# Kernel optimization log

Measured on AMD Instinct MI355X. Metric: run time of the kernel, lower is better.

## Reference

```python
import jax, jax.numpy as jnp
import numpy as np

P_IN = 32  # MODEL_CONFIG['p_in']; note: all 32 sample points share the same offsets in the source


def _bilinear_border(feat, sx, sy):
    """Replicates F.grid_sample(mode='bilinear', padding_mode='border', align_corners=False)
    for a single point per (b, n). feat: [B,C,H,W]; sx, sy: [B,N] in pixel coords.
    align_corners=False unnormalization of grid built as 2*s/size - 1 gives px = s - 0.5.
    Returns [B,N,C]."""
    H, W = feat.shape[-2], feat.shape[-1]
    px = jnp.clip(sx - 0.5, 0.0, W - 1.0)  # border padding clamps coords
    py = jnp.clip(sy - 0.5, 0.0, H - 1.0)
    x0 = jnp.floor(px)
    y0 = jnp.floor(py)
    wx = (px - x0)[..., None]  # [B,N,1]
    wy = (py - y0)[..., None]
    x0i = x0.astype(jnp.int32)
    y0i = y0.astype(jnp.int32)
    x1i = jnp.minimum(x0i + 1, W - 1)
    y1i = jnp.minimum(y0i + 1, H - 1)

    def gather(f, yi, xi):  # f [C,H,W], yi/xi [N] -> [N,C]
        return f[:, yi, xi].T

    g = jax.vmap(gather)  # over batch
    v00 = g(feat, y0i, x0i)
    v01 = g(feat, y0i, x1i)
    v10 = g(feat, y1i, x0i)
    v11 = g(feat, y1i, x1i)
    return (v00 * (1 - wx) * (1 - wy) + v01 * wx * (1 - wy)
            + v10 * (1 - wx) * wy + v11 * wx * wy)


def _forward(feats, query_pos, query_content, W_off, b_off, sigma_z):
    offsets = query_content @ W_off + b_off  # [B,N,3]
    x, y, z, r = (query_pos[..., i] for i in range(4))
    dx, dy, dz = offsets[..., 0], offsets[..., 1], offsets[..., 2]
    sx = x + dx * (2.0 ** (z - r))
    sy = y + dy * (2.0 ** (z + r))
    sz = z + dz
    L = len(feats)
    levels = jnp.arange(L, dtype=sz.dtype)
    # gaussian z weight, then softmax over levels (as in source: softmax of the exp values)
    w = jnp.exp(-((sz[..., None] - levels) ** 2) / (2.0 * sigma_z ** 2))  # [B,N,L]
    zw = jax.nn.softmax(w, axis=-1)
    out = sum(zw[..., l:l + 1] * _bilinear_border(feats[l], sx, sy) for l in range(L))  # [B,N,C]
    B, N, C = out.shape
    # all P_IN sample points use identical coords in the source -> broadcast
    return jnp.broadcast_to(out[:, :, None, :], (B, N, P_IN, C))


def setup_inputs() -> dict:
    key = jax.random.key(0)
    ks = jax.random.split(key, 8)
    B, N, C = 8, 300, 256
    sizes = [(100, 100), (50, 50), (25, 25), (13, 13)]
    feats = [jax.random.normal(ks[i], (B, C, h, w), dtype=jnp.float32)
             for i, (h, w) in enumerate(sizes)]
    u = jax.random.uniform(ks[4], (B, N, 4), dtype=jnp.float32)
    # x in [0,100), y in [0,100) (level-0 pixel coords), z in [0,4), r in [0,1)
    query_pos = u * jnp.array([100.0, 100.0, 4.0, 1.0], dtype=jnp.float32)
    query_content = jax.random.normal(ks[5], (B, N, C), dtype=jnp.float32)
    W_off = jax.random.normal(ks[6], (C, 3), dtype=jnp.float32) * 0.02
    b_off = jnp.zeros((3,), dtype=jnp.float32)
    sigma_z = jnp.ones((1,), dtype=jnp.float32) * 0.5
    return {"feat0": feats[0], "feat1": feats[1], "feat2": feats[2], "feat3": feats[3],
            "query_pos": query_pos, "query_content": query_content,
            "W_off": W_off, "b_off": b_off, "sigma_z": sigma_z}


def reference(feat0, feat1, feat2, feat3, query_pos, query_content, W_off, b_off, sigma_z):
    return _forward([feat0, feat1, feat2, feat3], query_pos, query_content, W_off, b_off, sigma_z)
```

## Files before the change

### kernel.cpp

```cpp
#include <hip/hip_runtime.h>

constexpr int Bc = 8;
constexpr int Nc = 300;
constexpr int Cc = 256;
constexpr int Pc = 32;

__global__ __launch_bounds__(256) void sampling3d_kernel(
    const float* __restrict__ f0, const float* __restrict__ f1,
    const float* __restrict__ f2, const float* __restrict__ f3,
    const float* __restrict__ qpos, const float* __restrict__ qcont,
    const float* __restrict__ Woff, const float* __restrict__ boff,
    const float* __restrict__ sigma, float* __restrict__ out)
{
    const int q = blockIdx.x;
    const int b = q / Nc;
    const int c = threadIdx.x;

    float qc = qcont[q * Cc + c];
    float p0 = qc * Woff[c * 3 + 0];
    float p1 = qc * Woff[c * 3 + 1];
    float p2 = qc * Woff[c * 3 + 2];
#pragma unroll
    for (int off = 32; off > 0; off >>= 1) {
        p0 += __shfl_down(p0, off, 64);
        p1 += __shfl_down(p1, off, 64);
        p2 += __shfl_down(p2, off, 64);
    }
    __shared__ float red[4][3];
    __shared__ float par[8];
    const int wave = threadIdx.x >> 6;
    const int lane = threadIdx.x & 63;
    if (lane == 0) { red[wave][0] = p0; red[wave][1] = p1; red[wave][2] = p2; }
    __syncthreads();
    if (threadIdx.x == 0) {
        float dx = red[0][0] + red[1][0] + red[2][0] + red[3][0] + boff[0];
        float dy = red[0][1] + red[1][1] + red[2][1] + red[3][1] + boff[1];
        float dz = red[0][2] + red[1][2] + red[2][2] + red[3][2] + boff[2];
        float x = qpos[q * 4 + 0];
        float y = qpos[q * 4 + 1];
        float z = qpos[q * 4 + 2];
        float r = qpos[q * 4 + 3];
        float sx = x + dx * exp2f(z - r);
        float sy = y + dy * exp2f(z + r);
        float sz = z + dz;
        float sg = sigma[0];
        float inv = 1.0f / (2.0f * sg * sg);
        float e[4];
        float s = 0.f;
#pragma unroll
        for (int l = 0; l < 4; ++l) {
            float d = sz - (float)l;
            float w = expf(-d * d * inv);
            e[l] = expf(w);
            s += e[l];
        }
        float rs = 1.0f / s;
        par[0] = sx;
        par[1] = sy;
#pragma unroll
        for (int l = 0; l < 4; ++l) par[2 + l] = e[l] * rs;
    }
    __syncthreads();

    const float sx = par[0];
    const float sy = par[1];

    const float* const fs[4] = {f0, f1, f2, f3};
    const int HWs[4] = {100, 50, 25, 13};

    float acc = 0.f;
#pragma unroll
    for (int l = 0; l < 4; ++l) {
        const int H = HWs[l];
        const int W = HWs[l];
        const float zw = par[2 + l];
        float px = fminf(fmaxf(sx - 0.5f, 0.f), (float)(W - 1));
        float py = fminf(fmaxf(sy - 0.5f, 0.f), (float)(H - 1));
        float x0f = floorf(px);
        float y0f = floorf(py);
        float wx = px - x0f;
        float wy = py - y0f;
        int x0 = (int)x0f;
        int y0 = (int)y0f;
        int x1 = min(x0 + 1, W - 1);
        int y1 = min(y0 + 1, H - 1);
        const float* base = fs[l] + (size_t)((b * Cc + c) * H) * W;
        float v00 = base[y0 * W + x0];
        float v01 = base[y0 * W + x1];
        float v10 = base[y1 * W + x0];
        float v11 = base[y1 * W + x1];
        float top = v00 + wx * (v01 - v00);
        float bot = v10 + wx * (v11 - v10);
        acc += zw * (top + wy * (bot - top));
    }

    float* o = out + (size_t)q * (Pc * Cc) + c;
#pragma unroll
    for (int p = 0; p < Pc; ++p) o[p * Cc] = acc;
}

extern "C" void kernel_launch(void* const* d_in, const int* in_sizes, int n_in,
                              void* d_out, int out_size, void* d_ws, size_t ws_size,
                              hipStream_t stream) {
    const float* f0    = (const float*)d_in[0];
    const float* f1    = (const float*)d_in[1];
    const float* f2    = (const float*)d_in[2];
    const float* f3    = (const float*)d_in[3];
    const float* qpos  = (const float*)d_in[4];
    const float* qcont = (const float*)d_in[5];
    const float* Woff  = (const float*)d_in[6];
    const float* boff  = (const float*)d_in[7];
    const float* sigma = (const float*)d_in[8];
    float* out = (float*)d_out;

    sampling3d_kernel<<<Bc * Nc, 256, 0, stream>>>(
        f0, f1, f2, f3, qpos, qcont, Woff, boff, sigma, out);
}
```

Baseline: 195.5 us.

## Split into params, LDS-staged per-channel sampling, and vectorized broadcast kernels

Splits the fused kernel into three launches. The first computes per-query sample coordinates and level weights into workspace. The second stages each (batch, channel) feature pyramid in LDS and samples all 300 queries from it, writing a transposed intermediate. The third broadcasts the result to the 32 sample points using 16-byte nontemporal stores. The aim is to replace scattered global gathers with LDS reads and to vectorize the large output write, at the cost of two extra launches, a workspace round-trip, and an original path kept as fallback.

```diff
diff --git a/kernel.cpp b/kernel.cpp
--- a/kernel.cpp
+++ b/kernel.cpp
@@ -5,17 +5,20 @@
 constexpr int Cc = 256;
 constexpr int Pc = 32;
 
-__global__ __launch_bounds__(256) void sampling3d_kernel(
-    const float* __restrict__ f0, const float* __restrict__ f1,
-    const float* __restrict__ f2, const float* __restrict__ f3,
+typedef float f32x4 __attribute__((ext_vector_type(4)));
+
+__constant__ int c_HW[4] = {100, 50, 25, 13};
+constexpr int LVL_N[4]   = {10000, 2500, 625, 169};
+constexpr int LVL_OFF[4] = {0, 10000, 12500, 13125};
+constexpr int LDS_FLOATS = 13294;
+
+__global__ __launch_bounds__(256) void params_kernel(
     const float* __restrict__ qpos, const float* __restrict__ qcont,
     const float* __restrict__ Woff, const float* __restrict__ boff,
-    const float* __restrict__ sigma, float* __restrict__ out)
+    const float* __restrict__ sigma, float* __restrict__ params)
 {
     const int q = blockIdx.x;
-    const int b = q / Nc;
     const int c = threadIdx.x;
-
     float qc = qcont[q * Cc + c];
     float p0 = qc * Woff[c * 3 + 0];
     float p1 = qc * Woff[c * 3 + 1];
@@ -27,10 +30,10 @@
         p2 += __shfl_down(p2, off, 64);
     }
     __shared__ float red[4][3];
-    __shared__ float par[8];
     const int wave = threadIdx.x >> 6;
-    const int lane = threadIdx.x & 63;
-    if (lane == 0) { red[wave][0] = p0; red[wave][1] = p1; red[wave][2] = p2; }
+    if ((threadIdx.x & 63) == 0) {
+        red[wave][0] = p0; red[wave][1] = p1; red[wave][2] = p2;
+    }
     __syncthreads();
     if (threadIdx.x == 0) {
         float dx = red[0][0] + red[1][0] + red[2][0] + red[3][0] + boff[0];
@@ -50,53 +53,186 @@
 #pragma unroll
         for (int l = 0; l < 4; ++l) {
             float d = sz - (float)l;
-            float w = expf(-d * d * inv);
-            e[l] = expf(w);
+            float w = __expf(-d * d * inv);
+            e[l] = __expf(w);
             s += e[l];
         }
         float rs = 1.0f / s;
-        par[0] = sx;
-        par[1] = sy;
+        params[q * 8 + 0] = sx;
+        params[q * 8 + 1] = sy;
+#pragma unroll
+        for (int l = 0; l < 4; ++l) params[q * 8 + 2 + l] = e[l] * rs;
+    }
+}
+
+__global__ __launch_bounds__(256) void sample_kernel(
+    const float* __restrict__ f0, const float* __restrict__ f1,
+    const float* __restrict__ f2, const float* __restrict__ f3,
+    const float* __restrict__ params, float* __restrict__ outT)
+{
+    __shared__ float sl[LDS_FLOATS];
+    const int bc = blockIdx.x;
+    const int t = threadIdx.x;
+
+    {
+        const f32x4* src = (const f32x4*)(f0 + (size_t)bc * 10000);
+        f32x4* dst = (f32x4*)&sl[LVL_OFF[0]];
+        for (int i = t; i < 2500; i += 256) dst[i] = src[i];
+    }
+    {
+        const f32x4* src = (const f32x4*)(f1 + (size_t)bc * 2500);
+        f32x4* dst = (f32x4*)&sl[LVL_OFF[1]];
+        for (int i = t; i < 625; i += 256) dst[i] = src[i];
+    }
+    {
+        const float* src = f2 + (size_t)bc * 625;
+        float* dst = &sl[LVL_OFF[2]];
+        for (int i = t; i < 625; i += 256) dst[i] = src[i];
+    }
+    {
+        const float* src = f3 + (size_t)bc * 169;
+        float* dst = &sl[LVL_OFF[3]];
+        if (t < 169) dst[t] = src[t];
+    }
+    __syncthreads();
+
+    const int b = bc >> 8;
+    for (int n = t; n < Nc; n += 256) {
+        const int q = b * Nc + n;
+        const float sx = params[q * 8 + 0];
+        const float sy = params[q * 8 + 1];
+        float acc = 0.f;
+#pragma unroll
+        for (int l = 0; l < 4; ++l) {
+            const int W = c_HW[l];
+            const float zw = params[q * 8 + 2 + l];
+            float px = fminf(fmaxf(sx - 0.5f, 0.f), (float)(W - 1));
+            float py = fminf(fmaxf(sy - 0.5f, 0.f), (float)(W - 1));
+            float x0f = floorf(px);
+            float y0f = floorf(py);
+            float wx = px - x0f;
+            float wy = py - y0f;
+            int x0 = (int)x0f;
+            int y0 = (int)y0f;
+            int x1 = min(x0 + 1, W - 1);
+            int y1 = min(y0 + 1, W - 1);
+            const float* base = &sl[LVL_OFF[l]];
+            float v00 = base[y0 * W + x0];
+            float v01 = base[y0 * W + x1];
+            float v10 = base[y1 * W + x0];
+            float v11 = base[y1 * W + x1];
+            float top = v00 + wx * (v01 - v00);
+            float bot = v10 + wx * (v11 - v10);
+            acc += zw * (top + wy * (bot - top));
+        }
+        outT[(size_t)bc * Nc + n] = acc;
+    }
+}
+
+__global__ __launch_bounds__(256) void broadcast_kernel(
+    const float* __restrict__ outT, float* __restrict__ out)
+{
+    __shared__ float sval[Cc];
+    const int q = blockIdx.x;
+    const int b = q / Nc;
+    const int n = q - b * Nc;
+    const int c = threadIdx.x;
+    sval[c] = outT[((size_t)(b * Cc + c)) * Nc + n];
+    __syncthreads();
+
+    const int wave = threadIdx.x >> 6;
+    const int c4 = (threadIdx.x & 63) * 4;
+    f32x4 val = *(const f32x4*)&sval[c4];
+    float* obase = out + (size_t)q * (Pc * Cc) + c4;
+#pragma unroll
+    for (int p = wave; p < Pc; p += 4) {
+        __builtin_nontemporal_store(val, (f32x4*)(obase + p * Cc));
+    }
+}
+
+__global__ __launch_bounds__(256) void sampling3d_fallback(
+    const float* __restrict__ f0, const float* __restrict__ f1,
+    const float* __restrict__ f2, const float* __restrict__ f3,
+    const float* __restrict__ qpos, const float* __restrict__ qcont,
+    const float* __restrict__ Woff, const float* __restrict__ boff,
+    const float* __restrict__ sigma, float* __restrict__ out)
+{
+    const int q = blockIdx.x;
+    const int b = q / Nc;
+    const int c = threadIdx.x;
+    float qc = qcont[q * Cc + c];
+    float p0 = qc * Woff[c * 3 + 0];
+    float p1 = qc * Woff[c * 3 + 1];
+    float p2 = qc * Woff[c * 3 + 2];
+#pragma unroll
+    for (int off = 32; off > 0; off >>= 1) {
+        p0 += __shfl_down(p0, off, 64);
+        p1 += __shfl_down(p1, off, 64);
+        p2 += __shfl_down(p2, off, 64);
+    }
+    __shared__ float red[4][3];
+    __shared__ float par[8];
+    __shared__ float accs[Cc];
+    const int wave = threadIdx.x >> 6;
+    if ((threadIdx.x & 63) == 0) { red[wave][0] = p0; red[wave][1] = p1; red[wave][2] = p2; }
+    __syncthreads();
+    if (threadIdx.x == 0) {
+        float dx = red[0][0] + red[1][0] + red[2][0] + red[3][0] + boff[0];
+        float dy = red[0][1] + red[1][1] + red[2][1] + red[3][1] + boff[1];
+        float dz = red[0][2] + red[1][2] + red[2][2] + red[3][2] + boff[2];
+        float x = qpos[q * 4 + 0], y = qpos[q * 4 + 1];
+        float z = qpos[q * 4 + 2], r = qpos[q * 4 + 3];
+        float sx = x + dx * exp2f(z - r);
+        float sy = y + dy * exp2f(z + r);
+        float sz = z + dz;
+        float sg = sigma[0];
+        float inv = 1.0f / (2.0f * sg * sg);
+        float e[4]; float s = 0.f;
+#pragma unroll
+        for (int l = 0; l < 4; ++l) {
+            float d = sz - (float)l;
+            float w = __expf(-d * d * inv);
+            e[l] = __expf(w);
+            s += e[l];
+        }
+        float rs = 1.0f / s;
+        par[0] = sx; par[1] = sy;
 #pragma unroll
         for (int l = 0; l < 4; ++l) par[2 + l] = e[l] * rs;
     }
     __syncthreads();
-
     const float sx = par[0];
     const float sy = par[1];
-
     const float* const fs[4] = {f0, f1, f2, f3};
     const int HWs[4] = {100, 50, 25, 13};
-
     float acc = 0.f;
 #pragma unroll
     for (int l = 0; l < 4; ++l) {
-        const int H = HWs[l];
         const int W = HWs[l];
-        const float zw = par[2 + l];
         float px = fminf(fmaxf(sx - 0.5f, 0.f), (float)(W - 1));
-        float py = fminf(fmaxf(sy - 0.5f, 0.f), (float)(H - 1));
-        float x0f = floorf(px);
-        float y0f = floorf(py);
-        float wx = px - x0f;
-        float wy = py - y0f;
-        int x0 = (int)x0f;
-        int y0 = (int)y0f;
-        int x1 = min(x0 + 1, W - 1);
-        int y1 = min(y0 + 1, H - 1);
-        const float* base = fs[l] + (size_t)((b * Cc + c) * H) * W;
+        float py = fminf(fmaxf(sy - 0.5f, 0.f), (float)(W - 1));
+        float x0f = floorf(px), y0f = floorf(py);
+        float wx = px - x0f, wy = py - y0f;
+        int x0 = (int)x0f, y0 = (int)y0f;
+        int x1 = min(x0 + 1, W - 1), y1 = min(y0 + 1, W - 1);
+        const float* base = fs[l] + (size_t)((b * Cc + c) * W) * W;
         float v00 = base[y0 * W + x0];
         float v01 = base[y0 * W + x1];
         float v10 = base[y1 * W + x0];
         float v11 = base[y1 * W + x1];
         float top = v00 + wx * (v01 - v00);
         float bot = v10 + wx * (v11 - v10);
-        acc += zw * (top + wy * (bot - top));
-    }
-
-    float* o = out + (size_t)q * (Pc * Cc) + c;
-#pragma unroll
-    for (int p = 0; p < Pc; ++p) o[p * Cc] = acc;
+        acc += par[2 + l] * (top + wy * (bot - top));
+    }
+    accs[c] = acc;
+    __syncthreads();
+    const int c4 = (threadIdx.x & 63) * 4;
+    f32x4 val = *(const f32x4*)&accs[c4];
+    float* obase = out + (size_t)q * (Pc * Cc) + c4;
+#pragma unroll
+    for (int p = wave; p < Pc; p += 4) {
+        __builtin_nontemporal_store(val, (f32x4*)(obase + p * Cc));
+    }
 }
 
 extern "C" void kernel_launch(void* const* d_in, const int* in_sizes, int n_in,
@@ -113,6 +249,17 @@
     const float* sigma = (const float*)d_in[8];
     float* out = (float*)d_out;
 
-    sampling3d_kernel<<<Bc * Nc, 256, 0, stream>>>(
-        f0, f1, f2, f3, qpos, qcont, Woff, boff, sigma, out);
-}
+    const size_t params_bytes = (size_t)Bc * Nc * 8 * sizeof(float);
+    const size_t outT_bytes   = (size_t)Bc * Cc * Nc * sizeof(float);
+
+    if (ws_size >= params_bytes + outT_bytes) {
+        float* params = (float*)d_ws;
+        float* outT   = (float*)((char*)d_ws + params_bytes);
+        params_kernel<<<Bc * Nc, 256, 0, stream>>>(qpos, qcont, Woff, boff, sigma, params);
+        sample_kernel<<<Bc * Cc, 256, 0, stream>>>(f0, f1, f2, f3, params, outT);
+        broadcast_kernel<<<Bc * Nc, 256, 0, stream>>>(outT, out);
+    } else {
+        sampling3d_fallback<<<Bc * Nc, 256, 0, stream>>>(
+            f0, f1, f2, f3, qpos, qcont, Woff, boff, sigma, out);
+    }
+}
```

Measured after the change: 198.9 us. About the same (+1.8%).
